# Optimization experiments

Measured on AMD Instinct MI355X. Metric: run time of the kernel, lower is better.

The kernel has to match this reference:

```python
import jax, jax.numpy as jnp
import numpy as np

EMBED_DIM = 1024
NUM_HEADS = 16
HEAD_DIM = EMBED_DIM // NUM_HEADS


def setup_inputs() -> dict:
    key = jax.random.key(0)
    k_x, k_wqkv, k_bqkv, k_wout, k_bout = jax.random.split(key, 5)
    B, T, C = 4, 2048, EMBED_DIM
    bound_qkv = 1.0 / np.sqrt(C)
    bound_out = 1.0 / np.sqrt(C)
    return {
        "x": jax.random.normal(k_x, (B, T, C), dtype=jnp.float32),
        # nn.Linear stores weight as [out, in]; we keep that convention.
        "w_qkv": jax.random.uniform(k_wqkv, (3 * C, C), jnp.float32, -bound_qkv, bound_qkv),
        "b_qkv": jax.random.uniform(k_bqkv, (3 * C,), jnp.float32, -bound_qkv, bound_qkv),
        "w_out": jax.random.uniform(k_wout, (C, C), jnp.float32, -bound_out, bound_out),
        "b_out": jax.random.uniform(k_bout, (C,), jnp.float32, -bound_out, bound_out),
    }


def reference(x, w_qkv, b_qkv, w_out, b_out):
    B, T, C = x.shape
    H, D = NUM_HEADS, HEAD_DIM
    qkv = x @ w_qkv.T + b_qkv                     # [B, T, 3C]
    qkv = qkv.reshape(B, T, 3, H, D)
    q = jnp.transpose(qkv[:, :, 0], (0, 2, 1, 3))  # [B, H, T, D]
    k = jnp.transpose(qkv[:, :, 1], (0, 2, 1, 3))
    v = jnp.transpose(qkv[:, :, 2], (0, 2, 1, 3))
    att = jnp.einsum('bhqd,bhkd->bhqk', q, k) / jnp.sqrt(jnp.float32(D))
    causal = jnp.tril(jnp.ones((T, T), dtype=bool))
    att = jnp.where(causal[None, None], att, -jnp.inf)
    att = jax.nn.softmax(att, axis=-1)
    # dropout p=0.0 (eval-mode identity)
    out = jnp.einsum('bhqk,bhkd->bhqd', att, v)    # [B, H, T, D]
    out = jnp.transpose(out, (0, 2, 1, 3)).reshape(B, T, C)
    return out @ w_out.T + b_out
```

## Files before the change

kernel.cpp:

```cpp
#include <hip/hip_runtime.h>
#include <hip/hip_bf16.h>


#define B_ 4
#define T_ 2048
#define C_ 1024
#define H_ 16
#define D_ 64
#define M_ (B_*T_)

#define SCALE_LOG2 0.18033688f

typedef __attribute__((ext_vector_type(8))) short short8;
typedef __attribute__((ext_vector_type(4))) float f32x4;
typedef __attribute__((ext_vector_type(16))) float f32x16;

static __device__ __forceinline__ ushort f2bf(float f) {
  __hip_bfloat16 b = __float2bfloat16(f);
  ushort u; __builtin_memcpy(&u, &b, 2); return u;
}

static __device__ __forceinline__ void ld16(const void* g, void* l) {
  __builtin_amdgcn_global_load_lds((const __attribute__((address_space(1))) void*)g,
                                   (__attribute__((address_space(3))) void*)l, 16, 0, 0);
}

static __device__ __forceinline__ f32x4 mfma16(short8 a, short8 b, f32x4 c) {
  return __builtin_amdgcn_mfma_f32_16x16x32_bf16(a, b, c, 0, 0, 0);
}
static __device__ __forceinline__ f32x16 mfma32(short8 a, short8 b, f32x16 c) {
  return __builtin_amdgcn_mfma_f32_32x32x16_bf16(a, b, c, 0, 0, 0);
}

static __device__ __forceinline__ float pair_max(float x) {
  return fmaxf(x, __shfl_xor(x, 32));
}
static __device__ __forceinline__ float pair_sum(float x) {
  return x + __shfl_xor(x, 32);
}

__global__ void cvt3(const float* __restrict__ a, const float* __restrict__ b,
                     const float* __restrict__ c, ushort* __restrict__ oa,
                     ushort* __restrict__ ob, ushort* __restrict__ oc,
                     int na, int nb, int nc) {
  int tot = na + nb + nc;
  int i = blockIdx.x * blockDim.x + threadIdx.x;
  int st = gridDim.x * blockDim.x;
  for (; i < tot; i += st) {
    const float* s; ushort* d; int k = i;
    if (k < na)            { s = a; d = oa; }
    else if (k < na + nb)  { k -= na; s = b; d = ob; }
    else                   { k -= na + nb; s = c; d = oc; }
    float4 v = ((const float4*)s)[k];
    ushort4 o;
    o.x = f2bf(v.x); o.y = f2bf(v.y); o.z = f2bf(v.z); o.w = f2bf(v.w);
    ((ushort4*)d)[k] = o;
  }
}

template<int MODE>
__global__ __launch_bounds__(256) void gemm_bt(
    const ushort* __restrict__ A, const ushort* __restrict__ Bm,
    const float* __restrict__ bias, int K,
    ushort* __restrict__ q, ushort* __restrict__ kk, ushort* __restrict__ vt,
    float* __restrict__ outF)
{
  __shared__ ushort SM[17408];
  const int tid = threadIdx.x;
  const int lane = tid & 63;
  const int w = tid >> 6;
  const int wr = w >> 1, wc = w & 1;
  const int l15 = lane & 15, lhi = lane >> 4;
  const long i0 = (long)blockIdx.y * 128;
  const long j0 = (long)blockIdx.x * 128;

  const int gsw = (lhi ^ ((l15 >> 1) & 3)) * 8;

  auto STAGE = [&](int buf, int k0) {
    int c = tid;
    int row = c >> 2, gs = (c & 3) ^ ((row >> 1) & 3);
    ld16((const char*)A  + ((i0 + row) * K + k0 + gs * 8) * 2, (char*)SM + buf*8192 + c*16);
    ld16((const char*)Bm + ((j0 + row) * K + k0 + gs * 8) * 2, (char*)SM + 16384 + buf*8192 + c*16);
    c = tid + 256;
    row = c >> 2; gs = (c & 3) ^ ((row >> 1) & 3);
    ld16((const char*)A  + ((i0 + row) * K + k0 + gs * 8) * 2, (char*)SM + buf*8192 + c*16);
    ld16((const char*)Bm + ((j0 + row) * K + k0 + gs * 8) * 2, (char*)SM + 16384 + buf*8192 + c*16);
  };

  f32x4 acc[4][4] = {};
  const int nsteps = K >> 5;

  STAGE(0, 0);
  STAGE(1, 32);
  int cur = 0;

  for (int t = 0; t < nsteps; t++) {
    if (t + 1 < nsteps) { asm volatile("s_waitcnt vmcnt(4)" ::: "memory"); }
    else                { asm volatile("s_waitcnt vmcnt(0)" ::: "memory"); }
    __builtin_amdgcn_s_barrier();
    __builtin_amdgcn_sched_barrier(0);

    short8 af[4], bf[4];
#pragma unroll
    for (int m = 0; m < 4; m++)
      af[m] = *(const short8*)&SM[cur*4096 + (wr*64 + m*16 + l15)*32 + gsw];
#pragma unroll
    for (int n = 0; n < 4; n++)
      bf[n] = *(const short8*)&SM[8192 + cur*4096 + (wc*64 + n*16 + l15)*32 + gsw];
    __builtin_amdgcn_s_setprio(1);
#pragma unroll
    for (int m = 0; m < 4; m++)
#pragma unroll
      for (int n = 0; n < 4; n++)
        acc[m][n] = mfma16(af[m], bf[n], acc[m][n]);
    __builtin_amdgcn_s_setprio(0);

    __builtin_amdgcn_s_barrier();
    __builtin_amdgcn_sched_barrier(0);
    if (t + 2 < nsteps) STAGE(cur, (t + 2) * 32);
    cur ^= 1;
  }

  if (MODE == 0 && j0 >= 2048) {
#pragma unroll
    for (int m = 0; m < 4; m++)
#pragma unroll
      for (int n = 0; n < 4; n++) {
        const int jl = wc*64 + n*16 + l15;
        const int tl = wr*64 + m*16 + lhi*4;
        const float bs = bias[j0 + jl];
        uint w0, w1;
        asm("v_cvt_pk_bf16_f32 %0, %1, %2" : "=v"(w0)
            : "v"(acc[m][n][0] + bs), "v"(acc[m][n][1] + bs));
        asm("v_cvt_pk_bf16_f32 %0, %1, %2" : "=v"(w1)
            : "v"(acc[m][n][2] + bs), "v"(acc[m][n][3] + bs));
        uint2 pr; pr.x = w0; pr.y = w1;
        *(uint2*)&SM[jl * 136 + tl] = pr;
      }
    __syncthreads();
    const int b = (int)(i0 >> 11);
    const int tb = (int)(i0 & 2047);
#pragma unroll
    for (int k2 = 0; k2 < 8; k2++) {
      const int chunk = k2 * 256 + tid;
      const int jl = chunk >> 4;
      const int t0 = (chunk & 15) * 8;
      uint4 pw = *(const uint4*)&SM[jl * 136 + t0];
      const int cc = (int)((j0 + jl) & 1023);
      const int h = cc >> 6, d = cc & 63;
      *(uint4*)&vt[((size_t)(b * H_ + h) * D_ + d) * T_ + tb + t0] = pw;
    }
  } else {
#pragma unroll
    for (int m = 0; m < 4; m++) {
#pragma unroll
      for (int n = 0; n < 4; n++) {
#pragma unroll
        for (int r = 0; r < 4; r++) {
          long i = i0 + wr*64 + m*16 + lhi*4 + r;
          int  j = (int)j0 + wc*64 + n*16 + l15;
          float v = acc[m][n][r] + bias[j];
          if (MODE == 0) {
            int b = (int)(i >> 11), t = (int)(i & 2047);
            int cc = j & 1023;
            int h = cc >> 6, d = cc & 63;
            long bh = (long)b * H_ + h;
            if (j < 1024)      q [(bh*T_ + t)*D_ + d] = f2bf(v * SCALE_LOG2);
            else               kk[(bh*T_ + t)*D_ + d] = f2bf(v);
          } else {
            outF[i * C_ + j] = v;
          }
        }
      }
    }
  }
}

#define PSTR 20

static __device__ __forceinline__ void softmax_pack32(
    f32x16& sc, float& m, float& lp, f32x16 (&o)[2],
    int q0, int kvbase, int l31, int hi, uint* __restrict__ P)
{
  float sv[16];
  const bool needmask = (kvbase + 31 > q0);
#pragma unroll
  for (int r = 0; r < 16; r++) {
    float xv = sc[r];
    if (needmask) {
      int kv = kvbase + (r & 3) + 8 * (r >> 2) + 4 * hi;
      if (kv > q0 + l31) xv = -1e30f;
    }
    sv[r] = xv;
  }
  float a0 = fmaxf(fmaxf(sv[0], sv[1]), sv[2]);
  float a1 = fmaxf(fmaxf(sv[3], sv[4]), sv[5]);
  float a2 = fmaxf(fmaxf(sv[6], sv[7]), sv[8]);
  float a3 = fmaxf(fmaxf(sv[9], sv[10]), sv[11]);
  float a4 = fmaxf(fmaxf(sv[12], sv[13]), sv[14]);
  float pmax = fmaxf(fmaxf(fmaxf(a0, a1), a2), fmaxf(fmaxf(a3, a4), sv[15]));
  if (__any(pmax > m + 8.0f)) {
    float rowm = pair_max(pmax);
    float nm = fmaxf(m, rowm);
    float alpha = __builtin_amdgcn_exp2f(m - nm);
    m = nm;
    lp *= alpha;
#pragma unroll
    for (int dt = 0; dt < 2; dt++)
#pragma unroll
      for (int r = 0; r < 16; r++) o[dt][r] *= alpha;
  }
  float s = 0.f;
#pragma unroll
  for (int r = 0; r < 16; r++) {
    float p = __builtin_amdgcn_exp2f(sv[r] - m);
    sv[r] = p;
    s += p;
  }
  lp += s;
  uint W[8];
#pragma unroll
  for (int r = 0; r < 8; r++)
    asm("v_cvt_pk_bf16_f32 %0, %1, %2" : "=v"(W[r]) : "v"(sv[2*r]), "v"(sv[2*r+1]));
#pragma unroll
  for (int r2 = 0; r2 < 4; r2++) {
    uint2 pr; pr.x = W[2*r2]; pr.y = W[2*r2 + 1];
    *(uint2*)&P[l31 * PSTR + r2*4 + 2*hi] = pr;
  }
}

__global__ __launch_bounds__(256, 2) void attn_k(
    const ushort* __restrict__ Q, const ushort* __restrict__ K,
    const ushort* __restrict__ V, ushort* __restrict__ AO)
{
  __shared__ ushort Kt[2][128*64];
  __shared__ ushort Vt[2][64*128];
  __shared__ uint P2[4][32 * PSTR];
  const int tid = threadIdx.x;
  const int lane = tid & 63;
  const int w = tid >> 6;
  const int l31 = lane & 31, hi = lane >> 5;
  const int bb = blockIdx.x;
  const int head = bb & 63;
  const int i = bb >> 6;
  const int J = (i < 4) ? i : 11 - i;
  const int nst = 16 - J;
  const int q0a = 128 * J + 32 * w;
  const int q0b = 2016 - 128 * J - 32 * w;

  const ushort* Qb = Q + (size_t)head * T_ * D_;
  const ushort* Kb = K + (size_t)head * T_ * D_;
  const ushort* Vb = V + (size_t)head * D_ * T_;

  auto STAGE = [&](int buf, int kv0s) {
#pragma unroll
    for (int hb = 0; hb < 4; hb++) {
      int slot = tid + hb * 256;
      int krow = slot >> 3, kg = slot & 7, kgs = kg ^ (krow & 7);
      ld16((const char*)Kb + ((size_t)(kv0s + krow) * D_ + kgs * 8) * 2,
           (char*)&Kt[buf][0] + slot * 16);
      int vrow = slot >> 4, vg = slot & 15, vgs = vg ^ (vrow & 15);
      ld16((const char*)Vb + ((size_t)vrow * T_ + kv0s + vgs * 8) * 2,
           (char*)&Vt[buf][0] + slot * 16);
    }
  };

  short8 qfa[4], qfb[4];
#pragma unroll
  for (int s = 0; s < 4; s++) {
    qfa[s] = *(const short8*)&Qb[(q0a + l31) * D_ + s*16 + hi*8];
    qfb[s] = *(const short8*)&Qb[(q0b + l31) * D_ + s*16 + hi*8];
  }

  f32x16 oa[2] = {}, ob[2] = {};
  float ma = -1e30f, la = 0.f, mb = -1e30f, lb = 0.f;

  STAGE(0, 0);
  STAGE(1, 128);
  int cur = 0;
  uint* P = &P2[w][0];

  for (int t = 0; t < nst; t++) {
    const int kv0 = t * 128;
    if (t + 1 < nst) { asm volatile("s_waitcnt vmcnt(8)" ::: "memory"); }
    else             { asm volatile("s_waitcnt vmcnt(0)" ::: "memory"); }
    __builtin_amdgcn_s_barrier();
    __builtin_amdgcn_sched_barrier(0);

#pragma unroll
    for (int c = 0; c < 4; c++) {
      const int kvc = kv0 + 32 * c;
      const bool act_b = (kvc <= q0b + 31);
      const bool act_a = (kvc <= q0a + 31);
      if (act_b) {
        short8 kf[4];
#pragma unroll
        for (int s = 0; s < 4; s++) {
          const int row = c*32 + l31;
          kf[s] = *(const short8*)&Kt[cur][row*64 + (((2*s + hi) ^ (row & 7)) << 3)];
        }
        short8 vf[2][2];
#pragma unroll
        for (int sl = 0; sl < 2; sl++)
#pragma unroll
          for (int dt = 0; dt < 2; dt++) {
            const int row = dt*32 + l31;
            const int u = c*4 + sl*2 + hi;
            vf[sl][dt] = *(const short8*)
                &Vt[cur][row*128 + ((u ^ (row & 15)) << 3)];
          }

        {
          f32x16 scb = {};
          __builtin_amdgcn_s_setprio(1);
#pragma unroll
          for (int s = 0; s < 4; s++) scb = mfma32(kf[s], qfb[s], scb);
          __builtin_amdgcn_s_setprio(0);
          softmax_pack32(scb, mb, lb, ob, q0b, kvc, l31, hi, P);
          asm volatile("s_waitcnt lgkmcnt(0)" ::: "memory");
          __builtin_amdgcn_sched_barrier(0);
          short8 pf[2];
#pragma unroll
          for (int sl = 0; sl < 2; sl++) {
            uint4 pw = *(const uint4*)&P[l31 * PSTR + sl*8 + hi*4];
            __builtin_memcpy(&pf[sl], &pw, 16);
          }
          __builtin_amdgcn_s_setprio(1);
#pragma unroll
          for (int sl = 0; sl < 2; sl++)
#pragma unroll
            for (int dt = 0; dt < 2; dt++)
              ob[dt] = mfma32(vf[sl][dt], pf[sl], ob[dt]);
          __builtin_amdgcn_s_setprio(0);
          __builtin_amdgcn_sched_barrier(0);
        }
        if (act_a) {
          f32x16 sca = {};
          __builtin_amdgcn_s_setprio(1);
#pragma unroll
          for (int s = 0; s < 4; s++) sca = mfma32(kf[s], qfa[s], sca);
          __builtin_amdgcn_s_setprio(0);
          softmax_pack32(sca, ma, la, oa, q0a, kvc, l31, hi, P);
          asm volatile("s_waitcnt lgkmcnt(0)" ::: "memory");
          __builtin_amdgcn_sched_barrier(0);
          short8 pf[2];
#pragma unroll
          for (int sl = 0; sl < 2; sl++) {
            uint4 pw = *(const uint4*)&P[l31 * PSTR + sl*8 + hi*4];
            __builtin_memcpy(&pf[sl], &pw, 16);
          }
          __builtin_amdgcn_s_setprio(1);
#pragma unroll
          for (int sl = 0; sl < 2; sl++)
#pragma unroll
            for (int dt = 0; dt < 2; dt++)
              oa[dt] = mfma32(vf[sl][dt], pf[sl], oa[dt]);
          __builtin_amdgcn_s_setprio(0);
          __builtin_amdgcn_sched_barrier(0);
        }
      }
    }

    __builtin_amdgcn_s_barrier();
    __builtin_amdgcn_sched_barrier(0);
    if (t + 2 < nst) STAGE(cur, kv0 + 256);
    cur ^= 1;
  }

  const int b = head >> 4, h = head & 15;
  {
    const float invl = 1.0f / pair_sum(lb);
    const size_t rowb = (size_t)(b * T_ + q0b + l31) * C_ + h * 64;
#pragma unroll
    for (int dt = 0; dt < 2; dt++)
#pragma unroll
      for (int rg = 0; rg < 4; rg++) {
        const int d0 = dt*32 + 8*rg + 4*hi;
        ushort4 ov;
        ov.x = f2bf(ob[dt][rg*4+0] * invl);
        ov.y = f2bf(ob[dt][rg*4+1] * invl);
        ov.z = f2bf(ob[dt][rg*4+2] * invl);
        ov.w = f2bf(ob[dt][rg*4+3] * invl);
        *(ushort4*)&AO[rowb + d0] = ov;
      }
  }
  {
    const float invl = 1.0f / pair_sum(la);
    const size_t rowb = (size_t)(b * T_ + q0a + l31) * C_ + h * 64;
#pragma unroll
    for (int dt = 0; dt < 2; dt++)
#pragma unroll
      for (int rg = 0; rg < 4; rg++) {
        const int d0 = dt*32 + 8*rg + 4*hi;
        ushort4 ov;
        ov.x = f2bf(oa[dt][rg*4+0] * invl);
        ov.y = f2bf(oa[dt][rg*4+1] * invl);
        ov.z = f2bf(oa[dt][rg*4+2] * invl);
        ov.w = f2bf(oa[dt][rg*4+3] * invl);
        *(ushort4*)&AO[rowb + d0] = ov;
      }
  }
}

extern "C" void kernel_launch(void* const* d_in, const int* in_sizes, int n_in,
                              void* d_out, int out_size, void* d_ws, size_t ws_size,
                              hipStream_t stream) {
  const float* x     = (const float*)d_in[0];
  const float* w_qkv = (const float*)d_in[1];
  const float* b_qkv = (const float*)d_in[2];
  const float* w_out = (const float*)d_in[3];
  const float* b_out = (const float*)d_in[4];
  float* out = (float*)d_out;

  ushort* xb    = (ushort*)d_ws;
  ushort* wqkvb = xb    + (size_t)M_ * C_;
  ushort* woutb = wqkvb + (size_t)3 * C_ * C_;
  ushort* q     = woutb + (size_t)C_ * C_;
  ushort* kk    = q     + (size_t)M_ * C_;
  ushort* vt    = kk    + (size_t)M_ * C_;
  ushort* ao    = xb;

  cvt3<<<2048, 256, 0, stream>>>(x, w_qkv, w_out, xb, wqkvb, woutb,
                                 (M_ * C_) / 4, (3 * C_ * C_) / 4, (C_ * C_) / 4);

  gemm_bt<0><<<dim3(3 * C_ / 128, M_ / 128), 256, 0, stream>>>(
      xb, wqkvb, b_qkv, C_, q, kk, vt, nullptr);

  attn_k<<<B_ * H_ * T_ / 256, 256, 0, stream>>>(q, kk, vt, ao);

  gemm_bt<1><<<dim3(C_ / 128, M_ / 128), 256, 0, stream>>>(
      ao, woutb, b_out, C_, nullptr, nullptr, nullptr, out);
}
```

Baseline: 171.0 us.

## Interleave both Q-tile softmax chains per KV chunk with separate P buffers

Issues the QK MFMAs for both query tiles back to back, then runs both softmaxes, writes both P tiles to separate LDS buffers, and does both PV MFMAs. The goal is to overlap MFMA latency with softmax VALU work across the two independent chains and to drop the explicit lgkmcnt waits and sched barriers between phases. The P row stride shrinks from 20 to 16 and the buffer count doubles. This raises register pressure, which may cause spills, and the smaller stride may bring LDS bank conflicts.

```diff
diff --git a/kernel.cpp b/kernel.cpp
--- a/kernel.cpp
+++ b/kernel.cpp
@@ -176,11 +176,11 @@
   }
 }
 
-#define PSTR 20
-
-static __device__ __forceinline__ void softmax_pack32(
+#define PSTR 16
+
+static __device__ __forceinline__ void sm_compute(
     f32x16& sc, float& m, float& lp, f32x16 (&o)[2],
-    int q0, int kvbase, int l31, int hi, uint* __restrict__ P)
+    int q0, int kvbase, int l31, int hi, uint (&W)[8])
 {
   float sv[16];
   const bool needmask = (kvbase + 31 > q0);
@@ -218,15 +218,9 @@
     s += p;
   }
   lp += s;
-  uint W[8];
 #pragma unroll
   for (int r = 0; r < 8; r++)
     asm("v_cvt_pk_bf16_f32 %0, %1, %2" : "=v"(W[r]) : "v"(sv[2*r]), "v"(sv[2*r+1]));
-#pragma unroll
-  for (int r2 = 0; r2 < 4; r2++) {
-    uint2 pr; pr.x = W[2*r2]; pr.y = W[2*r2 + 1];
-    *(uint2*)&P[l31 * PSTR + r2*4 + 2*hi] = pr;
-  }
 }
 
 __global__ __launch_bounds__(256, 2) void attn_k(
@@ -235,7 +229,7 @@
 {
   __shared__ ushort Kt[2][128*64];
   __shared__ ushort Vt[2][64*128];
-  __shared__ uint P2[4][32 * PSTR];
+  __shared__ uint P2[8][32 * PSTR];
   const int tid = threadIdx.x;
   const int lane = tid & 63;
   const int w = tid >> 6;
@@ -278,7 +272,8 @@
   STAGE(0, 0);
   STAGE(1, 128);
   int cur = 0;
-  uint* P = &P2[w][0];
+  uint* Pb = &P2[w*2][0];
+  uint* Pa = &P2[w*2+1][0];
 
   for (int t = 0; t < nst; t++) {
     const int kv0 = t * 128;
@@ -310,54 +305,60 @@
                 &Vt[cur][row*128 + ((u ^ (row & 15)) << 3)];
           }
 
-        {
-          f32x16 scb = {};
-          __builtin_amdgcn_s_setprio(1);
-#pragma unroll
-          for (int s = 0; s < 4; s++) scb = mfma32(kf[s], qfb[s], scb);
-          __builtin_amdgcn_s_setprio(0);
-          softmax_pack32(scb, mb, lb, ob, q0b, kvc, l31, hi, P);
-          asm volatile("s_waitcnt lgkmcnt(0)" ::: "memory");
-          __builtin_amdgcn_sched_barrier(0);
-          short8 pf[2];
+        f32x16 scb = {}, sca = {};
+        __builtin_amdgcn_s_setprio(1);
+#pragma unroll
+        for (int s = 0; s < 4; s++) scb = mfma32(kf[s], qfb[s], scb);
+        if (act_a) {
+#pragma unroll
+          for (int s = 0; s < 4; s++) sca = mfma32(kf[s], qfa[s], sca);
+        }
+        __builtin_amdgcn_s_setprio(0);
+
+        uint Wb[8], Wa[8];
+        sm_compute(scb, mb, lb, ob, q0b, kvc, l31, hi, Wb);
+        if (act_a) sm_compute(sca, ma, la, oa, q0a, kvc, l31, hi, Wa);
+
+#pragma unroll
+        for (int r2 = 0; r2 < 4; r2++) {
+          uint2 pr; pr.x = Wb[2*r2]; pr.y = Wb[2*r2 + 1];
+          *(uint2*)&Pb[l31 * PSTR + r2*4 + 2*hi] = pr;
+        }
+        if (act_a) {
+#pragma unroll
+          for (int r2 = 0; r2 < 4; r2++) {
+            uint2 pr; pr.x = Wa[2*r2]; pr.y = Wa[2*r2 + 1];
+            *(uint2*)&Pa[l31 * PSTR + r2*4 + 2*hi] = pr;
+          }
+        }
+        short8 pfb[2], pfa[2];
+#pragma unroll
+        for (int sl = 0; sl < 2; sl++) {
+          uint4 pw = *(const uint4*)&Pb[l31 * PSTR + sl*8 + hi*4];
+          __builtin_memcpy(&pfb[sl], &pw, 16);
+        }
+        if (act_a) {
 #pragma unroll
           for (int sl = 0; sl < 2; sl++) {
-            uint4 pw = *(const uint4*)&P[l31 * PSTR + sl*8 + hi*4];
-            __builtin_memcpy(&pf[sl], &pw, 16);
+            uint4 pw = *(const uint4*)&Pa[l31 * PSTR + sl*8 + hi*4];
+            __builtin_memcpy(&pfa[sl], &pw, 16);
           }
-          __builtin_amdgcn_s_setprio(1);
+        }
+
+        __builtin_amdgcn_s_setprio(1);
+#pragma unroll
+        for (int sl = 0; sl < 2; sl++)
+#pragma unroll
+          for (int dt = 0; dt < 2; dt++)
+            ob[dt] = mfma32(vf[sl][dt], pfb[sl], ob[dt]);
+        if (act_a) {
 #pragma unroll
           for (int sl = 0; sl < 2; sl++)
 #pragma unroll
             for (int dt = 0; dt < 2; dt++)
-              ob[dt] = mfma32(vf[sl][dt], pf[sl], ob[dt]);
-          __builtin_amdgcn_s_setprio(0);
-          __builtin_amdgcn_sched_barrier(0);
-        }
-        if (act_a) {
-          f32x16 sca = {};
-          __builtin_amdgcn_s_setprio(1);
-#pragma unroll
-          for (int s = 0; s < 4; s++) sca = mfma32(kf[s], qfa[s], sca);
-          __builtin_amdgcn_s_setprio(0);
-          softmax_pack32(sca, ma, la, oa, q0a, kvc, l31, hi, P);
-          asm volatile("s_waitcnt lgkmcnt(0)" ::: "memory");
-          __builtin_amdgcn_sched_barrier(0);
-          short8 pf[2];
-#pragma unroll
-          for (int sl = 0; sl < 2; sl++) {
-            uint4 pw = *(const uint4*)&P[l31 * PSTR + sl*8 + hi*4];
-            __builtin_memcpy(&pf[sl], &pw, 16);
-          }
-          __builtin_amdgcn_s_setprio(1);
-#pragma unroll
-          for (int sl = 0; sl < 2; sl++)
-#pragma unroll
-            for (int dt = 0; dt < 2; dt++)
-              oa[dt] = mfma32(vf[sl][dt], pf[sl], oa[dt]);
-          __builtin_amdgcn_s_setprio(0);
-          __builtin_amdgcn_sched_barrier(0);
-        }
+              oa[dt] = mfma32(vf[sl][dt], pfa[sl], oa[dt]);
+        }
+        __builtin_amdgcn_s_setprio(0);
       }
     }
 
```

After: 188.0 us. +9.9%, slower.
